# Performance work log

Measured on AMD Instinct MI355X. Metric: run time of the kernel, lower is better.

The kernel has to match this reference:

```python
import jax, jax.numpy as jnp
import numpy as np

N_TOKENS = 65536
D_MODEL = 1024
N_EXP = 64
TOP_K = 8
ROUTER_TEMP = 1.0  # select_temp=None -> selection uses router_temp
GUMBEL_TAU = 1.0   # unused: inference=True skips gumbel noise
EPS_T = 1e-06
EPS_D = 1e-09


def setup_inputs() -> dict:
    key = jax.random.key(0)
    k_h, k_w = jax.random.split(key)
    h = jax.random.normal(k_h, (N_TOKENS, D_MODEL), dtype=jnp.float32)
    # eqx.nn.Linear weight layout: [out_features, in_features] = [n_exp, d_model]
    W = jax.random.normal(k_w, (N_EXP, D_MODEL), dtype=jnp.float32) / np.sqrt(D_MODEL)
    token_mask = jnp.ones((N_TOKENS,), dtype=bool)
    return {"h": h, "W": W, "token_mask": token_mask}


def reference(h, W, token_mask):
    # inference=True path: no dropout, no gumbel noise.
    logits_clean = jnp.einsum("nd,ed->ne", h, W)  # [N, n_exp]

    # selection logits (select_temp defaults to router_temp)
    t_sel = jnp.clip(ROUTER_TEMP, EPS_T, None)
    logits_sel = logits_clean / t_sel
    logits_sel = jnp.where(token_mask[:, None], logits_sel, -jnp.inf)

    # top-k mask over experts
    _, idx = jax.lax.top_k(logits_sel, TOP_K)  # [N, k]
    n = logits_clean.shape[0]
    mask_full = jnp.zeros((n, N_EXP), dtype=bool).at[
        jnp.arange(n)[:, None], idx
    ].set(True)
    mask_full = mask_full & token_mask[:, None]

    # mixing probs: softmax(logits/T), zero masked tokens, renormalize over top-k
    t_mix = jnp.clip(ROUTER_TEMP, EPS_T, None)
    dense = jax.nn.softmax(logits_clean / t_mix, axis=-1)
    dense = jnp.where(token_mask[:, None], dense, 0.0)
    masked = jnp.where(mask_full, dense, 0.0)
    denom = jnp.clip(masked.sum(axis=-1, keepdims=True), EPS_D, None)
    probs = masked / denom
    probs = jnp.where(token_mask[:, None], probs, 0.0)

    return mask_full, probs, logits_clean, logits_sel
```

## Files before the change

kernel.cpp:

```cpp
#include <hip/hip_runtime.h>
#include <cmath>

#define NTOK 65536
#define DMOD 1024
#define NEXP 64
#define TOPK 8
#define BTOK 64
#define KCH  64
#define NCH  (DMOD / KCH)
#define STR  65

__device__ __forceinline__ bool tok_mask(const void* tm, int t, int mmode) {
    return mmode == 0 ? (((const unsigned char*)tm)[t] != 0)
                      : (((const unsigned int*)tm)[t] != 0u);
}

__global__ __launch_bounds__(256, 4)
void router_v10(const float* __restrict__ h,
                const float* __restrict__ W,
                const void* __restrict__ tmask,
                float* __restrict__ out)
{
    __shared__ float h_s[BTOK][STR];
    __shared__ float w_s[NEXP][STR];
    __shared__ float sm_m0[BTOK], sm_inv[BTOK];
    __shared__ unsigned long long mb[BTOK];

    const int tid  = threadIdx.x;
    const int lane = tid & 63;
    const int wave = tid >> 6;
    const int tg   = tid >> 3;
    const int eg   = tid & 7;
    const int t0   = blockIdx.x * BTOK;

    const unsigned int mw = *(const unsigned int*)tmask;
    const int mmode = (mw == 0x01010101u) ? 0 : 1;

    float acc[2][8];
#pragma unroll
    for (int i = 0; i < 2; ++i)
#pragma unroll
        for (int j = 0; j < 8; ++j) acc[i][j] = 0.f;

    const int sro = tid >> 4;
    const int sc  = (tid & 15) * 4;

    for (int c = 0; c < NCH; ++c) {
        const int kc = c * KCH;

        float4 ht[4], wt[4];
#pragma unroll
        for (int p = 0; p < 4; ++p) {
            const int row = p * 16 + sro;
            ht[p] = *reinterpret_cast<const float4*>(h + (size_t)(t0 + row) * DMOD + kc + sc);
            wt[p] = *reinterpret_cast<const float4*>(W + ((size_t)row << 10) + kc + sc);
        }
#pragma unroll
        for (int p = 0; p < 4; ++p) {
            const int row = p * 16 + sro;
            *reinterpret_cast<float4*>(&h_s[row][sc]) = ht[p];
            *reinterpret_cast<float4*>(&w_s[row][sc]) = wt[p];
        }
        __syncthreads();

#pragma unroll 4
        for (int k4 = 0; k4 < KCH / 4; ++k4) {
            float4 hv[2], wv[8];
#pragma unroll
            for (int i = 0; i < 2; ++i)
                hv[i] = *reinterpret_cast<const float4*>(&h_s[tg * 2 + i][k4 * 4]);
#pragma unroll
            for (int j = 0; j < 8; ++j)
                wv[j] = *reinterpret_cast<const float4*>(&w_s[eg * 8 + j][k4 * 4]);
#pragma unroll
            for (int i = 0; i < 2; ++i) {
#pragma unroll
                for (int j = 0; j < 8; ++j) {
                    float a = acc[i][j];
                    a = fmaf(hv[i].x, wv[j].x, a);
                    a = fmaf(hv[i].y, wv[j].y, a);
                    a = fmaf(hv[i].z, wv[j].z, a);
                    a = fmaf(hv[i].w, wv[j].w, a);
                    acc[i][j] = a;
                }
            }
        }
        __syncthreads();
    }

    float (*ls)[STR] = h_s;
#pragma unroll
    for (int i = 0; i < 2; ++i)
#pragma unroll
        for (int j = 0; j < 8; ++j)
            ls[tg * 2 + i][eg * 8 + j] = acc[i][j];

    __syncthreads();

    const size_t P = (size_t)NTOK * NEXP;
    float* __restrict__ o_mask = out;
    float* __restrict__ o_prob = out + P;
    float* __restrict__ o_lc   = out + 2 * P;
    float* __restrict__ o_lsl  = out + 3 * P;
    const size_t base = (size_t)t0 * NEXP;

#pragma unroll
    for (int p = 0; p < 4; ++p) {
        const int g  = p * 256 + tid;
        const int t  = g >> 4;
        const int e4 = (g & 15) * 4;
        const float4 lv = *reinterpret_cast<const float4*>(&ls[t][e4]);
        const bool tmt = tok_mask(tmask, t0 + t, mmode);
        float4 sv;
        sv.x = tmt ? lv.x : -INFINITY;
        sv.y = tmt ? lv.y : -INFINITY;
        sv.z = tmt ? lv.z : -INFINITY;
        sv.w = tmt ? lv.w : -INFINITY;
        *reinterpret_cast<float4*>(&o_lc[base + (size_t)g * 4])  = lv;
        *reinterpret_cast<float4*>(&o_lsl[base + (size_t)g * 4]) = sv;
    }

    if (wave == 0) {
        const int lt = lane;
        const bool tm = tok_mask(tmask, t0 + lt, mmode);

        unsigned long long bits = 0ULL;
        float m0 = -INFINITY;
        for (int r = 0; r < TOPK; ++r) {
            float bv = -INFINITY; int bi = 0;
            for (int e = 0; e < 64; ++e) {
                if ((bits >> e) & 1ULL) continue;
                const float x = ls[lt][e];
                if (x > bv) { bv = x; bi = e; }
            }
            bits |= 1ULL << bi;
            if (r == 0) m0 = bv;
        }

        float ssum = 0.f;
        for (int e = 0; e < 64; ++e)
            if ((bits >> e) & 1ULL) ssum += expf(ls[lt][e] - m0);

        sm_m0[lt]  = m0;
        sm_inv[lt] = 1.0f / ssum;
        mb[lt] = tm ? bits : 0ULL;
    }

    __syncthreads();

#pragma unroll
    for (int p = 0; p < 4; ++p) {
        const int g  = p * 256 + tid;
        const int t  = g >> 4;
        const int e4 = (g & 15) * 4;
        const float4 lv = *reinterpret_cast<const float4*>(&ls[t][e4]);
        const unsigned long long bt = mb[t];
        const float m0 = sm_m0[t], inv = sm_inv[t];
        float4 pv, mv;
        const bool s0 = (bt >> (e4 + 0)) & 1ULL;
        const bool s1 = (bt >> (e4 + 1)) & 1ULL;
        const bool s2 = (bt >> (e4 + 2)) & 1ULL;
        const bool s3 = (bt >> (e4 + 3)) & 1ULL;
        pv.x = s0 ? expf(lv.x - m0) * inv : 0.f;
        pv.y = s1 ? expf(lv.y - m0) * inv : 0.f;
        pv.z = s2 ? expf(lv.z - m0) * inv : 0.f;
        pv.w = s3 ? expf(lv.w - m0) * inv : 0.f;
        mv.x = s0 ? 1.f : 0.f;
        mv.y = s1 ? 1.f : 0.f;
        mv.z = s2 ? 1.f : 0.f;
        mv.w = s3 ? 1.f : 0.f;
        *reinterpret_cast<float4*>(&o_prob[base + (size_t)g * 4]) = pv;
        *reinterpret_cast<float4*>(&o_mask[base + (size_t)g * 4]) = mv;
    }
}

extern "C" void kernel_launch(void* const* d_in, const int* in_sizes, int n_in,
                              void* d_out, int out_size, void* d_ws, size_t ws_size,
                              hipStream_t stream)
{
    const float* h = (const float*)d_in[0];
    const float* W = (const float*)d_in[1];
    const void*  tmask = (const void*)d_in[2];
    float* out = (float*)d_out;

    hipLaunchKernelGGL(router_v10, dim3(NTOK / BTOK), dim3(256), 0, stream,
                       h, W, tmask, out);
}
```

Measured before the change: 283.7 us.

## Double token tile and read router weights directly from global/L2 instead of LDS

Token tile per block grows from 64 to 128 and each thread now computes a 4x8 tile instead of 2x8. The shared-memory copy of W is dropped, and each thread loads its 8 expert weight rows straight from global memory, relying on cache since W is shared by every block. The goal is to cut LDS traffic and staging work and to raise arithmetic per LDS load. The cost is more registers (launch bounds lowered to 2 blocks per CU), half as many blocks, and many uncoalesced-per-thread global loads of W inside the inner loop.

```diff
diff --git a/kernel.cpp b/kernel.cpp
--- a/kernel.cpp
+++ b/kernel.cpp
@@ -5,7 +5,7 @@
 #define DMOD 1024
 #define NEXP 64
 #define TOPK 8
-#define BTOK 64
+#define BTOK 128
 #define KCH  64
 #define NCH  (DMOD / KCH)
 #define STR  65
@@ -15,65 +15,67 @@
                       : (((const unsigned int*)tm)[t] != 0u);
 }
 
-__global__ __launch_bounds__(256, 4)
-void router_v10(const float* __restrict__ h,
+__global__ __launch_bounds__(256, 2)
+void router_v12(const float* __restrict__ h,
                 const float* __restrict__ W,
                 const void* __restrict__ tmask,
                 float* __restrict__ out)
 {
     __shared__ float h_s[BTOK][STR];
-    __shared__ float w_s[NEXP][STR];
     __shared__ float sm_m0[BTOK], sm_inv[BTOK];
     __shared__ unsigned long long mb[BTOK];
 
     const int tid  = threadIdx.x;
     const int lane = tid & 63;
     const int wave = tid >> 6;
-    const int tg   = tid >> 3;
-    const int eg   = tid & 7;
+    const int tt   = tid & 15;
+    const int ee   = ((tid >> 4) & 3) | (((tid >> 6) & 1) << 2);
+    const int half = tid >> 7;
+    const int trow = half * 64 + tt * 4;
     const int t0   = blockIdx.x * BTOK;
 
     const unsigned int mw = *(const unsigned int*)tmask;
     const int mmode = (mw == 0x01010101u) ? 0 : 1;
 
-    float acc[2][8];
+    const float* __restrict__ wrow = W + ((size_t)(ee * 8) << 10);
+
+    float acc[4][8];
 #pragma unroll
-    for (int i = 0; i < 2; ++i)
+    for (int i = 0; i < 4; ++i)
 #pragma unroll
         for (int j = 0; j < 8; ++j) acc[i][j] = 0.f;
 
-    const int sro = tid >> 4;
-    const int sc  = (tid & 15) * 4;
+    const int sr = tid >> 4;
+    const int sc = (tid & 15) * 4;
 
     for (int c = 0; c < NCH; ++c) {
         const int kc = c * KCH;
 
-        float4 ht[4], wt[4];
+        float4 ht[8];
 #pragma unroll
-        for (int p = 0; p < 4; ++p) {
-            const int row = p * 16 + sro;
+        for (int p = 0; p < 8; ++p) {
+            const int row = p * 16 + sr;
             ht[p] = *reinterpret_cast<const float4*>(h + (size_t)(t0 + row) * DMOD + kc + sc);
-            wt[p] = *reinterpret_cast<const float4*>(W + ((size_t)row << 10) + kc + sc);
         }
 #pragma unroll
-        for (int p = 0; p < 4; ++p) {
-            const int row = p * 16 + sro;
+        for (int p = 0; p < 8; ++p) {
+            const int row = p * 16 + sr;
             *reinterpret_cast<float4*>(&h_s[row][sc]) = ht[p];
-            *reinterpret_cast<float4*>(&w_s[row][sc]) = wt[p];
         }
         __syncthreads();
 
-#pragma unroll 4
+#pragma unroll
         for (int k4 = 0; k4 < KCH / 4; ++k4) {
-            float4 hv[2], wv[8];
+            float4 hv[4];
 #pragma unroll
-            for (int i = 0; i < 2; ++i)
-                hv[i] = *reinterpret_cast<const float4*>(&h_s[tg * 2 + i][k4 * 4]);
+            for (int i = 0; i < 4; ++i)
+                hv[i] = *reinterpret_cast<const float4*>(&h_s[trow + i][k4 * 4]);
+            float4 wv[8];
 #pragma unroll
             for (int j = 0; j < 8; ++j)
-                wv[j] = *reinterpret_cast<const float4*>(&w_s[eg * 8 + j][k4 * 4]);
+                wv[j] = *reinterpret_cast<const float4*>(wrow + ((size_t)j << 10) + kc + k4 * 4);
 #pragma unroll
-            for (int i = 0; i < 2; ++i) {
+            for (int i = 0; i < 4; ++i) {
 #pragma unroll
                 for (int j = 0; j < 8; ++j) {
                     float a = acc[i][j];
@@ -90,10 +92,10 @@
 
     float (*ls)[STR] = h_s;
 #pragma unroll
-    for (int i = 0; i < 2; ++i)
+    for (int i = 0; i < 4; ++i)
 #pragma unroll
         for (int j = 0; j < 8; ++j)
-            ls[tg * 2 + i][eg * 8 + j] = acc[i][j];
+            ls[trow + i][ee * 8 + j] = acc[i][j];
 
     __syncthreads();
 
@@ -105,7 +107,7 @@
     const size_t base = (size_t)t0 * NEXP;
 
 #pragma unroll
-    for (int p = 0; p < 4; ++p) {
+    for (int p = 0; p < 8; ++p) {
         const int g  = p * 256 + tid;
         const int t  = g >> 4;
         const int e4 = (g & 15) * 4;
@@ -120,8 +122,8 @@
         *reinterpret_cast<float4*>(&o_lsl[base + (size_t)g * 4]) = sv;
     }
 
-    if (wave == 0) {
-        const int lt = lane;
+    if (wave < 2) {
+        const int lt = wave * 64 + lane;
         const bool tm = tok_mask(tmask, t0 + lt, mmode);
 
         unsigned long long bits = 0ULL;
@@ -149,7 +151,7 @@
     __syncthreads();
 
 #pragma unroll
-    for (int p = 0; p < 4; ++p) {
+    for (int p = 0; p < 8; ++p) {
         const int g  = p * 256 + tid;
         const int t  = g >> 4;
         const int e4 = (g & 15) * 4;
@@ -183,6 +185,6 @@
     const void*  tmask = (const void*)d_in[2];
     float* out = (float*)d_out;
 
-    hipLaunchKernelGGL(router_v10, dim3(NTOK / BTOK), dim3(256), 0, stream,
+    hipLaunchKernelGGL(router_v12, dim3(NTOK / BTOK), dim3(256), 0, stream,
                        h, W, tmask, out);
 }
```

Measured after the change: 619.3 us. +118.3%, slower.

## Halve K-chunk, reshape thread tile to 4x4, raise occupancy target

Applied to the files above, without the earlier changes.

Cuts the shared-memory K chunk from 64 to 32 and aliases the logits staging buffer onto the same shared array, shrinking shared memory per block. Launch bounds move from 4 to 8 blocks per SM so more waves can hide global-load latency. Each thread's register tile changes from 2 tokens x 8 experts to 4x4, which cuts LDS vector reads per k-step from 10 to 8. The trade-off is twice as many chunk iterations and barriers, plus tighter register limits from the higher occupancy target.

```diff
diff --git a/kernel.cpp b/kernel.cpp
--- a/kernel.cpp
+++ b/kernel.cpp
@@ -6,76 +6,76 @@
 #define NEXP 64
 #define TOPK 8
 #define BTOK 64
-#define KCH  64
+#define KCH  32
 #define NCH  (DMOD / KCH)
-#define STR  65
+#define TSTR 33
+#define LSTR 65
 
 __device__ __forceinline__ bool tok_mask(const void* tm, int t, int mmode) {
     return mmode == 0 ? (((const unsigned char*)tm)[t] != 0)
                       : (((const unsigned int*)tm)[t] != 0u);
 }
 
-__global__ __launch_bounds__(256, 4)
-void router_v10(const float* __restrict__ h,
+__global__ __launch_bounds__(256, 8)
+void router_v14(const float* __restrict__ h,
                 const float* __restrict__ W,
                 const void* __restrict__ tmask,
                 float* __restrict__ out)
 {
-    __shared__ float h_s[BTOK][STR];
-    __shared__ float w_s[NEXP][STR];
+    __shared__ __align__(16) float smem[2 * 64 * TSTR];
     __shared__ float sm_m0[BTOK], sm_inv[BTOK];
     __shared__ unsigned long long mb[BTOK];
+
+    float (*h_s)[TSTR] = reinterpret_cast<float(*)[TSTR]>(smem);
+    float (*w_s)[TSTR] = reinterpret_cast<float(*)[TSTR]>(smem + 64 * TSTR);
+    float (*ls)[LSTR]  = reinterpret_cast<float(*)[LSTR]>(smem);
 
     const int tid  = threadIdx.x;
     const int lane = tid & 63;
     const int wave = tid >> 6;
-    const int tg   = tid >> 3;
-    const int eg   = tid & 7;
+    const int tt   = tid & 15;
+    const int ee   = tid >> 4;
     const int t0   = blockIdx.x * BTOK;
 
     const unsigned int mw = *(const unsigned int*)tmask;
     const int mmode = (mw == 0x01010101u) ? 0 : 1;
 
-    float acc[2][8];
+    float acc[4][4];
 #pragma unroll
-    for (int i = 0; i < 2; ++i)
+    for (int i = 0; i < 4; ++i)
 #pragma unroll
-        for (int j = 0; j < 8; ++j) acc[i][j] = 0.f;
+        for (int j = 0; j < 4; ++j) acc[i][j] = 0.f;
 
-    const int sro = tid >> 4;
-    const int sc  = (tid & 15) * 4;
+    const int sr0 = tid >> 3;
+    const int sr1 = (256 + tid) >> 3;
+    const int sc  = (tid & 7) * 4;
 
     for (int c = 0; c < NCH; ++c) {
         const int kc = c * KCH;
 
-        float4 ht[4], wt[4];
-#pragma unroll
-        for (int p = 0; p < 4; ++p) {
-            const int row = p * 16 + sro;
-            ht[p] = *reinterpret_cast<const float4*>(h + (size_t)(t0 + row) * DMOD + kc + sc);
-            wt[p] = *reinterpret_cast<const float4*>(W + ((size_t)row << 10) + kc + sc);
-        }
-#pragma unroll
-        for (int p = 0; p < 4; ++p) {
-            const int row = p * 16 + sro;
-            *reinterpret_cast<float4*>(&h_s[row][sc]) = ht[p];
-            *reinterpret_cast<float4*>(&w_s[row][sc]) = wt[p];
-        }
+        const float4 ha = *reinterpret_cast<const float4*>(h + (size_t)(t0 + sr0) * DMOD + kc + sc);
+        const float4 hb = *reinterpret_cast<const float4*>(h + (size_t)(t0 + sr1) * DMOD + kc + sc);
+        const float4 wa = *reinterpret_cast<const float4*>(W + ((size_t)sr0 << 10) + kc + sc);
+        const float4 wb = *reinterpret_cast<const float4*>(W + ((size_t)sr1 << 10) + kc + sc);
+        *reinterpret_cast<float4*>(&h_s[sr0][sc]) = ha;
+        *reinterpret_cast<float4*>(&h_s[sr1][sc]) = hb;
+        *reinterpret_cast<float4*>(&w_s[sr0][sc]) = wa;
+        *reinterpret_cast<float4*>(&w_s[sr1][sc]) = wb;
         __syncthreads();
 
-#pragma unroll 4
+#pragma unroll
         for (int k4 = 0; k4 < KCH / 4; ++k4) {
-            float4 hv[2], wv[8];
+            float4 hv[4], wv[4];
 #pragma unroll
-            for (int i = 0; i < 2; ++i)
-                hv[i] = *reinterpret_cast<const float4*>(&h_s[tg * 2 + i][k4 * 4]);
+            for (int i = 0; i < 4; ++i)
+                hv[i] = *reinterpret_cast<const float4*>(&h_s[tt * 4 + i][k4 * 4]);
 #pragma unroll
-            for (int j = 0; j < 8; ++j)
-                wv[j] = *reinterpret_cast<const float4*>(&w_s[eg * 8 + j][k4 * 4]);
+            for (int j = 0; j < 4; ++j)
+                wv[j] = *reinterpret_cast<const float4*>(&w_s[ee * 4 + j][k4 * 4]);
 #pragma unroll
-            for (int i = 0; i < 2; ++i) {
+            for (int i = 0; i < 4; ++i) {
 #pragma unroll
-                for (int j = 0; j < 8; ++j) {
+                for (int j = 0; j < 4; ++j) {
                     float a = acc[i][j];
                     a = fmaf(hv[i].x, wv[j].x, a);
                     a = fmaf(hv[i].y, wv[j].y, a);
@@ -88,12 +88,11 @@
         __syncthreads();
     }
 
-    float (*ls)[STR] = h_s;
 #pragma unroll
-    for (int i = 0; i < 2; ++i)
+    for (int i = 0; i < 4; ++i)
 #pragma unroll
-        for (int j = 0; j < 8; ++j)
-            ls[tg * 2 + i][eg * 8 + j] = acc[i][j];
+        for (int j = 0; j < 4; ++j)
+            ls[tt * 4 + i][ee * 4 + j] = acc[i][j];
 
     __syncthreads();
 
@@ -183,6 +182,6 @@
     const void*  tmask = (const void*)d_in[2];
     float* out = (float*)d_out;
 
-    hipLaunchKernelGGL(router_v10, dim3(NTOK / BTOK), dim3(256), 0, stream,
+    hipLaunchKernelGGL(router_v14, dim3(NTOK / BTOK), dim3(256), 0, stream,
                        h, W, tmask, out);
 }
```

After: 696.2 us. +145.4%, slower.
